# Kernel tuning notes

Measured on AMD Instinct MI355X. Metric: run time of the kernel, lower is better.

## Reference

```python
import jax, jax.numpy as jnp
import numpy as np

L1, L2, N, C = 4096, 4096, 8, 3


def setup_inputs() -> dict:
    key = jax.random.key(0)
    k1, k2 = jax.random.split(key)
    coords1 = jax.random.uniform(k1, (L1, N, C), dtype=jnp.float32)
    coords2 = jax.random.uniform(k2, (L2, N, C), dtype=jnp.float32)
    return {"coords1": coords1, "coords2": coords2}


def reference(coords1, coords2):
    # coords1: [L1, N, C], coords2: [L2, N, C]
    l1, n, c = coords1.shape
    l2 = coords2.shape[0]
    # Batch-first layout, matching flatten_batch semantics (per-batch NN only)
    q = jnp.swapaxes(coords2, 0, 1)  # [N, L2, C] query points
    r = jnp.swapaxes(coords1, 0, 1)  # [N, L1, C] reference points
    # Squared euclidean distances per batch: [N, L2, L1]
    d2 = (
        jnp.sum(q * q, axis=-1)[:, :, None]
        + jnp.sum(r * r, axis=-1)[:, None, :]
        - 2.0 * jnp.einsum("nlc,nmc->nlm", q, r)
    )
    # tc.nearest returns global flat index; original does fmod(L1) to get the
    # per-batch index — argmin within each batch gives that directly.
    nearest = jnp.argmin(d2, axis=-1)  # [N, L2]
    clusters = nearest.T  # [L2, N]
    # torch.meshgrid(arange(L2), arange(N)) with 'ij' indexing; indices[-1] is
    # the batch index broadcast to [L2, N].
    batch_idx = jnp.broadcast_to(jnp.arange(n, dtype=jnp.int64 if False else jnp.int32), (l2, n))
    return (clusters.reshape(-1), batch_idx.reshape(-1))
```

## Files before the change

### kernel.cpp

```cpp
#include <hip/hip_runtime.h>
#include <float.h>


typedef float v2f __attribute__((ext_vector_type(2)));

constexpr int kL1 = 4096, kL2 = 4096, kN = 8;
constexpr int kChunk = 1024;
constexpr int kQPerBlock = 16;
constexpr int kQ = 4;

__device__ __forceinline__ v2f dist_pk(v2f qx, v2f qy, v2f qz, v2f qq,
                                       v2f r01, v2f r23, v2f n2) {
  v2f d, t;
  asm("v_pk_mul_f32 %0, %2, %6 op_sel:[0,0] op_sel_hi:[1,0]\n\t"
      "v_pk_mul_f32 %1, %3, %6 op_sel:[0,1] op_sel_hi:[1,1]\n\t"
      "v_pk_add_f32 %0, %0, %1\n\t"
      "v_pk_mul_f32 %1, %4, %7 op_sel:[0,0] op_sel_hi:[1,0]\n\t"
      "v_pk_add_f32 %0, %0, %1\n\t"
      "v_pk_add_f32 %1, %5, %7 op_sel:[0,1] op_sel_hi:[1,1]\n\t"
      "v_pk_fma_f32 %0, %0, %8, %1"
      : "=&v"(d), "=&v"(t)
      : "v"(qx), "v"(qy), "v"(qz), "v"(qq), "v"(r01), "v"(r23), "v"(n2));
  return d;
}

__global__ __launch_bounds__(256, 4)
void nearest_kernel(const float* __restrict__ c1, const float* __restrict__ c2,
                    int* __restrict__ out) {
#pragma clang fp contract(off)
  __shared__ float4 refs[4][256];

  const int tid = threadIdx.x;
  const int n = blockIdx.y;
  const int wave = tid >> 6;
  const int lane = tid & 63;
  const int q0 = blockIdx.x * kQPerBlock + wave * kQ;

  float qxs[kQ], qys[kQ], qzs[kQ], qqs[kQ];
#pragma unroll
  for (int i = 0; i < kQ; ++i) {
    const float* p = c2 + ((q0 + i) * kN + n) * 3;
    qxs[i] = p[0]; qys[i] = p[1]; qzs[i] = p[2];
    qqs[i] = __fadd_rn(__fadd_rn(__fmul_rn(qxs[i], qxs[i]), __fmul_rn(qys[i], qys[i])),
                       __fmul_rn(qzs[i], qzs[i]));
  }
  const v2f qx01 = {qxs[0], qxs[1]}, qx23 = {qxs[2], qxs[3]};
  const v2f qy01 = {qys[0], qys[1]}, qy23 = {qys[2], qys[3]};
  const v2f qz01 = {qzs[0], qzs[1]}, qz23 = {qzs[2], qzs[3]};
  const v2f qq01 = {qqs[0], qqs[1]}, qq23 = {qqs[2], qqs[3]};
  const v2f n2 = {-2.0f, -2.0f};

  float bd[kQ]; int bt[kQ];
#pragma unroll
  for (int i = 0; i < kQ; ++i) { bd[i] = FLT_MAX; bt[i] = 0; }

  int tg = 0;
  for (int chunk = 0; chunk < kL1 / kChunk; ++chunk) {
    __syncthreads();

    {
      const int jb = chunk * kChunk + tid * 4;
#pragma unroll
      for (int k = 0; k < 4; ++k) {
        const float3 rp = *reinterpret_cast<const float3*>(c1 + ((jb + k) * kN + n) * 3);
        const float rr = __fadd_rn(
            __fadd_rn(__fmul_rn(rp.x, rp.x), __fmul_rn(rp.y, rp.y)),
            __fmul_rn(rp.z, rp.z));
        refs[k][tid] = make_float4(rp.x, rp.y, rp.z, rr);
      }
    }
    __syncthreads();

#pragma unroll
    for (int t = 0; t < kChunk / 256; ++t, ++tg) {
      const float4 rA = refs[0][t * 64 + lane];
      const float4 rB = refs[1][t * 64 + lane];
      const float4 rC = refs[2][t * 64 + lane];
      const float4 rD = refs[3][t * 64 + lane];

      const v2f dA01 = dist_pk(qx01, qy01, qz01, qq01, (v2f){rA.x, rA.y}, (v2f){rA.z, rA.w}, n2);
      const v2f dA23 = dist_pk(qx23, qy23, qz23, qq23, (v2f){rA.x, rA.y}, (v2f){rA.z, rA.w}, n2);
      const v2f dB01 = dist_pk(qx01, qy01, qz01, qq01, (v2f){rB.x, rB.y}, (v2f){rB.z, rB.w}, n2);
      const v2f dB23 = dist_pk(qx23, qy23, qz23, qq23, (v2f){rB.x, rB.y}, (v2f){rB.z, rB.w}, n2);
      const v2f dC01 = dist_pk(qx01, qy01, qz01, qq01, (v2f){rC.x, rC.y}, (v2f){rC.z, rC.w}, n2);
      const v2f dC23 = dist_pk(qx23, qy23, qz23, qq23, (v2f){rC.x, rC.y}, (v2f){rC.z, rC.w}, n2);
      const v2f dD01 = dist_pk(qx01, qy01, qz01, qq01, (v2f){rD.x, rD.y}, (v2f){rD.z, rD.w}, n2);
      const v2f dD23 = dist_pk(qx23, qy23, qz23, qq23, (v2f){rD.x, rD.y}, (v2f){rD.z, rD.w}, n2);

      const float m0 = fminf(fminf(dA01.x, dB01.x), fminf(dC01.x, dD01.x));
      const float m1 = fminf(fminf(dA01.y, dB01.y), fminf(dC01.y, dD01.y));
      const float m2 = fminf(fminf(dA23.x, dB23.x), fminf(dC23.x, dD23.x));
      const float m3 = fminf(fminf(dA23.y, dB23.y), fminf(dC23.y, dD23.y));
      if (m0 < bd[0]) { bd[0] = m0; bt[0] = tg; }
      if (m1 < bd[1]) { bd[1] = m1; bt[1] = tg; }
      if (m2 < bd[2]) { bd[2] = m2; bt[2] = tg; }
      if (m3 < bd[3]) { bd[3] = m3; bt[3] = tg; }
    }
  }

  int sel[kQ];
#pragma unroll
  for (int i = 0; i < kQ; ++i) sel[i] = bt[i] * 64 + lane;
#pragma unroll
  for (int m = 1; m <= 32; m <<= 1) {
#pragma unroll
    for (int i = 0; i < kQ; ++i) {
      const float od = __shfl_xor(bd[i], m);
      const int os = __shfl_xor(sel[i], m);
      if (od < bd[i] || (od == bd[i] && os < sel[i])) { bd[i] = od; sel[i] = os; }
    }
  }

#pragma unroll
  for (int i = 0; i < kQ; ++i) {
    if (lane == i) {
      const int j0 = sel[i] * 4;
      float dc[4];
#pragma unroll
      for (int k = 0; k < 4; ++k) {
        const float3 rp = *reinterpret_cast<const float3*>(c1 + ((j0 + k) * kN + n) * 3);
        const float rr = __fadd_rn(
            __fadd_rn(__fmul_rn(rp.x, rp.x), __fmul_rn(rp.y, rp.y)),
            __fmul_rn(rp.z, rp.z));
        const float dot = __fadd_rn(
            __fadd_rn(__fmul_rn(qxs[i], rp.x), __fmul_rn(qys[i], rp.y)),
            __fmul_rn(qzs[i], rp.z));
        dc[k] = __fmaf_rn(-2.0f, dot, __fadd_rn(qqs[i], rr));
      }
      int kk = 3;
      if (dc[2] == bd[i]) kk = 2;
      if (dc[1] == bd[i]) kk = 1;
      if (dc[0] == bd[i]) kk = 0;
      out[(q0 + i) * kN + n] = j0 + kk;
      out[kL2 * kN + (q0 + i) * kN + n] = n;
    }
  }
}

extern "C" void kernel_launch(void* const* d_in, const int* in_sizes, int n_in,
                              void* d_out, int out_size, void* d_ws, size_t ws_size,
                              hipStream_t stream) {
  const float* c1 = (const float*)d_in[0];
  const float* c2 = (const float*)d_in[1];
  int* out = (int*)d_out;
  dim3 grid(kL2 / kQPerBlock, kN);
  nearest_kernel<<<grid, dim3(256), 0, stream>>>(c1, c2, out);
}
```

Measured before the change: 99.19 us.

## Switch ref tile to SoA shared layout and vectorize over ref pairs

Stores reference coordinates in shared memory as separate x/y/z/norm arrays and loads four consecutive refs per lane as float4. Packed math now pairs two references against one broadcast query, instead of pairing two queries against one reference. The min update folds into fminf, with a conditional index write. The goal is cleaner packed-op operands without op_sel tricks and fewer LDS instructions, at the cost of extra broadcast query registers. The final tie-break is rewritten to pick the first minimum.

```diff
diff --git a/kernel.cpp b/kernel.cpp
--- a/kernel.cpp
+++ b/kernel.cpp
@@ -9,26 +9,29 @@
 constexpr int kQPerBlock = 16;
 constexpr int kQ = 4;
 
-__device__ __forceinline__ v2f dist_pk(v2f qx, v2f qy, v2f qz, v2f qq,
-                                       v2f r01, v2f r23, v2f n2) {
-  v2f d, t;
-  asm("v_pk_mul_f32 %0, %2, %6 op_sel:[0,0] op_sel_hi:[1,0]\n\t"
-      "v_pk_mul_f32 %1, %3, %6 op_sel:[0,1] op_sel_hi:[1,1]\n\t"
-      "v_pk_add_f32 %0, %0, %1\n\t"
-      "v_pk_mul_f32 %1, %4, %7 op_sel:[0,0] op_sel_hi:[1,0]\n\t"
-      "v_pk_add_f32 %0, %0, %1\n\t"
-      "v_pk_add_f32 %1, %5, %7 op_sel:[0,1] op_sel_hi:[1,1]\n\t"
-      "v_pk_fma_f32 %0, %0, %8, %1"
-      : "=&v"(d), "=&v"(t)
-      : "v"(qx), "v"(qy), "v"(qz), "v"(qq), "v"(r01), "v"(r23), "v"(n2));
-  return d;
+__device__ __forceinline__ v2f pk_mul(v2f a, v2f b) {
+  v2f d; asm("v_pk_mul_f32 %0, %1, %2" : "=v"(d) : "v"(a), "v"(b)); return d;
+}
+__device__ __forceinline__ v2f pk_add(v2f a, v2f b) {
+  v2f d; asm("v_pk_add_f32 %0, %1, %2" : "=v"(d) : "v"(a), "v"(b)); return d;
+}
+__device__ __forceinline__ v2f pk_fma(v2f a, v2f b, v2f c) {
+  v2f d; asm("v_pk_fma_f32 %0, %1, %2, %3" : "=v"(d) : "v"(a), "v"(b), "v"(c)); return d;
+}
+
+__device__ __forceinline__ v2f dist2_pair(v2f qx, v2f qy, v2f qz, v2f qq,
+                                          v2f rx, v2f ry, v2f rz, v2f rr, v2f n2) {
+  const v2f s01 = pk_add(pk_mul(qx, rx), pk_mul(qy, ry));
+  const v2f dot = pk_add(s01, pk_mul(qz, rz));
+  const v2f A = pk_add(qq, rr);
+  return pk_fma(dot, n2, A);
 }
 
 __global__ __launch_bounds__(256, 4)
 void nearest_kernel(const float* __restrict__ c1, const float* __restrict__ c2,
                     int* __restrict__ out) {
 #pragma clang fp contract(off)
-  __shared__ float4 refs[4][256];
+  __shared__ float sRx[kChunk], sRy[kChunk], sRz[kChunk], sRr[kChunk];
 
   const int tid = threadIdx.x;
   const int n = blockIdx.y;
@@ -37,64 +40,69 @@
   const int q0 = blockIdx.x * kQPerBlock + wave * kQ;
 
   float qxs[kQ], qys[kQ], qzs[kQ], qqs[kQ];
+  v2f qx2[kQ], qy2[kQ], qz2[kQ], qq2[kQ];
 #pragma unroll
   for (int i = 0; i < kQ; ++i) {
     const float* p = c2 + ((q0 + i) * kN + n) * 3;
     qxs[i] = p[0]; qys[i] = p[1]; qzs[i] = p[2];
     qqs[i] = __fadd_rn(__fadd_rn(__fmul_rn(qxs[i], qxs[i]), __fmul_rn(qys[i], qys[i])),
                        __fmul_rn(qzs[i], qzs[i]));
+    qx2[i] = (v2f){qxs[i], qxs[i]};
+    qy2[i] = (v2f){qys[i], qys[i]};
+    qz2[i] = (v2f){qzs[i], qzs[i]};
+    qq2[i] = (v2f){qqs[i], qqs[i]};
   }
-  const v2f qx01 = {qxs[0], qxs[1]}, qx23 = {qxs[2], qxs[3]};
-  const v2f qy01 = {qys[0], qys[1]}, qy23 = {qys[2], qys[3]};
-  const v2f qz01 = {qzs[0], qzs[1]}, qz23 = {qzs[2], qzs[3]};
-  const v2f qq01 = {qqs[0], qqs[1]}, qq23 = {qqs[2], qqs[3]};
   const v2f n2 = {-2.0f, -2.0f};
 
   float bd[kQ]; int bt[kQ];
 #pragma unroll
   for (int i = 0; i < kQ; ++i) { bd[i] = FLT_MAX; bt[i] = 0; }
 
-  int tg = 0;
   for (int chunk = 0; chunk < kL1 / kChunk; ++chunk) {
     __syncthreads();
 
     {
       const int jb = chunk * kChunk + tid * 4;
+      float x[4], y[4], z[4], w4[4];
 #pragma unroll
       for (int k = 0; k < 4; ++k) {
-        const float3 rp = *reinterpret_cast<const float3*>(c1 + ((jb + k) * kN + n) * 3);
-        const float rr = __fadd_rn(
-            __fadd_rn(__fmul_rn(rp.x, rp.x), __fmul_rn(rp.y, rp.y)),
-            __fmul_rn(rp.z, rp.z));
-        refs[k][tid] = make_float4(rp.x, rp.y, rp.z, rr);
+        const float* p = c1 + ((jb + k) * kN + n) * 3;
+        x[k] = p[0]; y[k] = p[1]; z[k] = p[2];
+        w4[k] = __fadd_rn(__fadd_rn(__fmul_rn(x[k], x[k]), __fmul_rn(y[k], y[k])),
+                          __fmul_rn(z[k], z[k]));
       }
+      *reinterpret_cast<float4*>(&sRx[tid * 4]) = make_float4(x[0], x[1], x[2], x[3]);
+      *reinterpret_cast<float4*>(&sRy[tid * 4]) = make_float4(y[0], y[1], y[2], y[3]);
+      *reinterpret_cast<float4*>(&sRz[tid * 4]) = make_float4(z[0], z[1], z[2], z[3]);
+      *reinterpret_cast<float4*>(&sRr[tid * 4]) = make_float4(w4[0], w4[1], w4[2], w4[3]);
     }
     __syncthreads();
 
 #pragma unroll
-    for (int t = 0; t < kChunk / 256; ++t, ++tg) {
-      const float4 rA = refs[0][t * 64 + lane];
-      const float4 rB = refs[1][t * 64 + lane];
-      const float4 rC = refs[2][t * 64 + lane];
-      const float4 rD = refs[3][t * 64 + lane];
+    for (int t = 0; t < kChunk / 256; ++t) {
+      const int tg = chunk * (kChunk / 256) + t;
+      const int base = t * 256 + lane * 4;
+      const float4 rx4 = *reinterpret_cast<const float4*>(&sRx[base]);
+      const float4 ry4 = *reinterpret_cast<const float4*>(&sRy[base]);
+      const float4 rz4 = *reinterpret_cast<const float4*>(&sRz[base]);
+      const float4 rr4 = *reinterpret_cast<const float4*>(&sRr[base]);
+      const v2f rx01 = {rx4.x, rx4.y}, rx23 = {rx4.z, rx4.w};
+      const v2f ry01 = {ry4.x, ry4.y}, ry23 = {ry4.z, ry4.w};
+      const v2f rz01 = {rz4.x, rz4.y}, rz23 = {rz4.z, rz4.w};
+      const v2f rr01 = {rr4.x, rr4.y}, rr23 = {rr4.z, rr4.w};
 
-      const v2f dA01 = dist_pk(qx01, qy01, qz01, qq01, (v2f){rA.x, rA.y}, (v2f){rA.z, rA.w}, n2);
-      const v2f dA23 = dist_pk(qx23, qy23, qz23, qq23, (v2f){rA.x, rA.y}, (v2f){rA.z, rA.w}, n2);
-      const v2f dB01 = dist_pk(qx01, qy01, qz01, qq01, (v2f){rB.x, rB.y}, (v2f){rB.z, rB.w}, n2);
-      const v2f dB23 = dist_pk(qx23, qy23, qz23, qq23, (v2f){rB.x, rB.y}, (v2f){rB.z, rB.w}, n2);
-      const v2f dC01 = dist_pk(qx01, qy01, qz01, qq01, (v2f){rC.x, rC.y}, (v2f){rC.z, rC.w}, n2);
-      const v2f dC23 = dist_pk(qx23, qy23, qz23, qq23, (v2f){rC.x, rC.y}, (v2f){rC.z, rC.w}, n2);
-      const v2f dD01 = dist_pk(qx01, qy01, qz01, qq01, (v2f){rD.x, rD.y}, (v2f){rD.z, rD.w}, n2);
-      const v2f dD23 = dist_pk(qx23, qy23, qz23, qq23, (v2f){rD.x, rD.y}, (v2f){rD.z, rD.w}, n2);
-
-      const float m0 = fminf(fminf(dA01.x, dB01.x), fminf(dC01.x, dD01.x));
-      const float m1 = fminf(fminf(dA01.y, dB01.y), fminf(dC01.y, dD01.y));
-      const float m2 = fminf(fminf(dA23.x, dB23.x), fminf(dC23.x, dD23.x));
-      const float m3 = fminf(fminf(dA23.y, dB23.y), fminf(dC23.y, dD23.y));
-      if (m0 < bd[0]) { bd[0] = m0; bt[0] = tg; }
-      if (m1 < bd[1]) { bd[1] = m1; bt[1] = tg; }
-      if (m2 < bd[2]) { bd[2] = m2; bt[2] = tg; }
-      if (m3 < bd[3]) { bd[3] = m3; bt[3] = tg; }
+#pragma unroll
+      for (int i = 0; i < kQ; ++i) {
+        const v2f d01 = dist2_pair(qx2[i], qy2[i], qz2[i], qq2[i],
+                                   rx01, ry01, rz01, rr01, n2);
+        const v2f d23 = dist2_pair(qx2[i], qy2[i], qz2[i], qq2[i],
+                                   rx23, ry23, rz23, rr23, n2);
+        const float old = bd[i];
+        float m = fminf(fminf(d01.x, d01.y), old);
+        m = fminf(fminf(d23.x, d23.y), m);
+        bd[i] = m;
+        if (m < old) bt[i] = tg;
+      }
     }
   }
 
@@ -115,22 +123,19 @@
   for (int i = 0; i < kQ; ++i) {
     if (lane == i) {
       const int j0 = sel[i] * 4;
-      float dc[4];
+      float best = FLT_MAX; int kk = 0;
 #pragma unroll
       for (int k = 0; k < 4; ++k) {
-        const float3 rp = *reinterpret_cast<const float3*>(c1 + ((j0 + k) * kN + n) * 3);
+        const float* p = c1 + ((j0 + k) * kN + n) * 3;
+        const float r0 = p[0], r1 = p[1], r2 = p[2];
         const float rr = __fadd_rn(
-            __fadd_rn(__fmul_rn(rp.x, rp.x), __fmul_rn(rp.y, rp.y)),
-            __fmul_rn(rp.z, rp.z));
+            __fadd_rn(__fmul_rn(r0, r0), __fmul_rn(r1, r1)), __fmul_rn(r2, r2));
         const float dot = __fadd_rn(
-            __fadd_rn(__fmul_rn(qxs[i], rp.x), __fmul_rn(qys[i], rp.y)),
-            __fmul_rn(qzs[i], rp.z));
-        dc[k] = __fmaf_rn(-2.0f, dot, __fadd_rn(qqs[i], rr));
+            __fadd_rn(__fmul_rn(qxs[i], r0), __fmul_rn(qys[i], r1)),
+            __fmul_rn(qzs[i], r2));
+        const float dc = __fmaf_rn(-2.0f, dot, __fadd_rn(qqs[i], rr));
+        if (dc < best) { best = dc; kk = k; }
       }
-      int kk = 3;
-      if (dc[2] == bd[i]) kk = 2;
-      if (dc[1] == bd[i]) kk = 1;
-      if (dc[0] == bd[i]) kk = 0;
       out[(q0 + i) * kN + n] = j0 + kk;
       out[kL2 * kN + (q0 + i) * kN + n] = n;
     }
```

Measured after the change: 99.80 us. No clear change (+0.6%).
